# Kernel optimization log

Measured on AMD Instinct MI355X. Metric: run time of the kernel, lower is better.

## Reference

```python
import jax, jax.numpy as jnp
import numpy as np

B, D, N, E = 4, 128, 16384, 65536  # batch, feature_dim, n_junctions, 2*n_lines
EPS = 1e-5  # BatchNorm eps


def setup_inputs() -> dict:
    key = jax.random.key(0)
    ks = jax.random.split(key, 8)
    s = lambda k, shape: jax.random.normal(k, shape, dtype=jnp.float32)
    return {
        "ldesc0": s(ks[0], (B, D, N)),
        "ldesc1": s(ks[1], (B, D, N)),
        "line_enc0": s(ks[2], (B, D, E)),
        "line_enc1": s(ks[3], (B, D, E)),
        "lines_junc_idx0": jax.random.randint(ks[4], (B, E), 0, N),
        "lines_junc_idx1": jax.random.randint(ks[5], (B, E), 0, N),
        # MLP([3D, 2D, D]) params: conv1x1 -> BN -> ReLU -> conv1x1
        "w1": s(ks[6], (2 * D, 3 * D)) * 0.05,
        "b1": jnp.zeros((2 * D,), jnp.float32),
        "bn_gamma": jnp.ones((2 * D,), jnp.float32),
        "bn_beta": jnp.zeros((2 * D,), jnp.float32),
        "bn_mean": jnp.zeros((2 * D,), jnp.float32),
        "bn_var": jnp.ones((2 * D,), jnp.float32),
        "w2": s(ks[7], (D, 2 * D)) * 0.05,
        "b2": jnp.zeros((D,), jnp.float32),
    }


def _mlp(x, w1, b1, g, beta, mu, var, w2, b2):
    # x: [B, 3D, E] -> [B, D, E]; BN in inference mode with running stats
    h = jnp.einsum('oi,bie->boe', w1, x) + b1[None, :, None]
    scale = g / jnp.sqrt(var + EPS)
    h = h * scale[None, :, None] + (beta - mu * scale)[None, :, None]
    h = jax.nn.relu(h)
    return jnp.einsum('oi,bie->boe', w2, h) + b2[None, :, None]


def _endpoint_update(ldesc, line_enc, idx, params):
    # gather endpoint descriptors: [B, D, E]
    line_desc = jax.vmap(lambda x, i: x[:, i])(ldesc, idx)
    b, d, e = line_desc.shape
    # swap the two endpoints of each line (flip along the size-2 axis)
    flipped = line_desc.reshape(b, d, e // 2, 2)[..., ::-1].reshape(b, d, e)
    message = jnp.concatenate([line_desc, flipped, line_enc], axis=1)  # [B, 3D, E]
    return _mlp(message, *params)


def _scatter_mean(src, idx, n):
    # src: [B, D, E], idx: [B, E] -> mean-reduced [B, D, n]; empty slots stay 0
    def one(s, i):
        sums = jax.ops.segment_sum(s.T, i, num_segments=n)                    # [n, D]
        cnt = jax.ops.segment_sum(jnp.ones(s.shape[1], s.dtype), i, num_segments=n)
        return (sums / jnp.maximum(cnt, 1.0)[:, None]).T                      # [D, n]
    return jax.vmap(one)(src, idx)


def reference(ldesc0, ldesc1, line_enc0, line_enc1, lines_junc_idx0, lines_junc_idx1,
              w1, b1, bn_gamma, bn_beta, bn_mean, bn_var, w2, b2):
    params = (w1, b1, bn_gamma, bn_beta, bn_mean, bn_var, w2, b2)
    up0 = _endpoint_update(ldesc0, line_enc0, lines_junc_idx0, params)
    up1 = _endpoint_update(ldesc1, line_enc1, lines_junc_idx1, params)
    n = ldesc0.shape[2]
    out0 = ldesc0 + _scatter_mean(up0, lines_junc_idx0, n)
    out1 = ldesc1 + _scatter_mean(up1, lines_junc_idx1, n)
    return (out0, out1)
```

## Files before the change

### kernel.cpp

```cpp
#include <hip/hip_runtime.h>
#include <hip/hip_bf16.h>
#include <stdint.h>

#define Bb 4
#define Dd 128
#define Nn 16384
#define Ee 65536
#define NTB 16

typedef __attribute__((ext_vector_type(4))) float f32x4;
typedef __attribute__((ext_vector_type(8))) short s16x8;

__device__ __forceinline__ unsigned short f2bf(float f) {
  union { float f; unsigned int u; } v; v.f = f;
  unsigned int r = v.u + 0x7fffu + ((v.u >> 16) & 1u);
  return (unsigned short)(r >> 16);
}

__device__ __forceinline__ unsigned int cvtpk(float lo, float hi) {
  unsigned int r;
  asm volatile("v_cvt_pk_bf16_f32 %0, %1, %2" : "=v"(r) : "v"(lo), "v"(hi));
  return r;
}

__global__ void prep_weights(const float* __restrict__ w1, const float* __restrict__ b1,
                             const float* __restrict__ g, const float* __restrict__ beta,
                             const float* __restrict__ mu, const float* __restrict__ var,
                             const float* __restrict__ w2,
                             unsigned short* __restrict__ W1s, unsigned short* __restrict__ W2s,
                             float* __restrict__ c1) {
  int i = blockIdx.x * 256 + threadIdx.x;
  if (i < 256 * 384) {
    int o = i / 384;
    float scale = g[o] * rsqrtf(var[o] + 1e-5f);
    W1s[i] = f2bf(w1[i] * scale);
  }
  if (i < 128 * 256) W2s[i] = f2bf(w2[i]);
  if (i < 256) {
    float scale = g[i] * rsqrtf(var[i] + 1e-5f);
    c1[i] = b1[i] * scale + beta[i] - mu[i] * scale;
  }
}

__global__ void transpose_ldesc(const float* __restrict__ l0, const float* __restrict__ l1,
                                unsigned short* __restrict__ dst, int side0) {
  __shared__ float tile[32][33];
  int z = blockIdx.z;
  int gs = side0 + (z >> 2), b = z & 3;
  const float* src = (gs ? l1 : l0) + (size_t)b * Dd * Nn;
  unsigned short* d = dst + (size_t)z * Nn * Dd;
  int n0 = blockIdx.x * 32;
  int d0 = blockIdx.y * 32;
  int tx = threadIdx.x, ty = threadIdx.y;
#pragma unroll
  for (int i = 0; i < 4; ++i)
    tile[ty + i * 8][tx] = src[(size_t)(d0 + ty + i * 8) * Nn + n0 + tx];
  __syncthreads();
#pragma unroll
  for (int i = 0; i < 4; ++i) {
    int r = ty + i * 8;
    d[(size_t)(n0 + r) * Dd + d0 + tx] = f2bf(tile[tx][r]);
  }
}

__global__ void hist_kernel(const int* __restrict__ idx0, const int* __restrict__ idx1,
                            int* __restrict__ hist) {
  int i = blockIdx.x * 256 + threadIdx.x;
  int sb = i >> 16;
  int e = i & 65535;
  const int* jx = (sb >= 4) ? idx1 : idx0;
  int n = jx[(size_t)(sb & 3) * Ee + e];
  atomicAdd(&hist[sb * Nn + n], 1);
}

__global__ __launch_bounds__(1024) void scan_kernel(const int* __restrict__ hist,
                                                    int* __restrict__ offs,
                                                    int* __restrict__ cursor) {
  __shared__ int part[1024];
  int sb = blockIdx.x, t = threadIdx.x;
  const int* h = hist + sb * Nn;
  int base = t * 16;
  int v[16];
  int local = 0;
#pragma unroll
  for (int i = 0; i < 16; ++i) { v[i] = local; local += h[base + i]; }
  part[t] = local;
  __syncthreads();
  for (int d = 1; d < 1024; d <<= 1) {
    int y = (t >= d) ? part[t - d] : 0;
    __syncthreads();
    part[t] += y;
    __syncthreads();
  }
  int excl = part[t] - local;
#pragma unroll
  for (int i = 0; i < 16; ++i) {
    int o = excl + v[i];
    offs[sb * Nn + base + i] = o;
    cursor[sb * Nn + base + i] = o;
  }
}

__global__ void fill_kernel(const int* __restrict__ idx0, const int* __restrict__ idx1,
                            int* __restrict__ cursor, int* __restrict__ perm) {
  int i = blockIdx.x * 256 + threadIdx.x;
  int sb = i >> 16;
  int e = i & 65535;
  const int* jx = (sb >= 4) ? idx1 : idx0;
  int n = jx[(size_t)(sb & 3) * Ee + e];
  int pos = atomicAdd(&cursor[sb * Nn + n], 1);
  perm[(size_t)sb * Ee + e] = pos;
}

#define STAGE_DESC(ti, buf)                                                     \
  do {                                                                          \
    int e0s_ = (tile0 + (ti)) * 64;                                             \
    unsigned char* xb_ = sm + (buf) * 32768;                                    \
    int cA_ = w * 8 + (lane >> 4);                                              \
    int cB_ = cA_ + 4;                                                          \
    int uA_ = (lane & 15) ^ (cA_ & 7);                                          \
    int uB_ = (lane & 15) ^ (cB_ & 7);                                          \
    int iA_ = jxB[e0s_ + cA_];                                                  \
    int iB_ = jxB[e0s_ + cB_];                                                  \
    __builtin_amdgcn_global_load_lds(                                           \
        (const __attribute__((address_space(1))) void*)(ldB + ((size_t)iA_) * 128 + uA_ * 8), \
        (__attribute__((address_space(3))) void*)(xb_ + (w * 8) * 256), 16, 0, 0); \
    __builtin_amdgcn_global_load_lds(                                           \
        (const __attribute__((address_space(1))) void*)(ldB + ((size_t)iB_) * 128 + uB_ * 8), \
        (__attribute__((address_space(3))) void*)(xb_ + (w * 8 + 4) * 256), 16, 0, 0); \
  } while (0)

#define ENC_LOAD(ti)                                                            \
  do {                                                                          \
    int e0s_ = (tile0 + (ti)) * 64;                                             \
    const float* es_ = enF + (size_t)(oct * 8) * Ee + e0s_ + ep * 2;            \
    _Pragma("unroll") for (int r = 0; r < 8; ++r)                               \
      ereg[r] = *(const float2*)(es_ + (size_t)r * Ee);                         \
  } while (0)

#define ENC_WRITE(buf)                                                          \
  do {                                                                          \
    unsigned char* xb_ = sm + (buf) * 32768;                                    \
    _Pragma("unroll") for (int j = 0; j < 2; ++j) {                             \
      int e_ = ep * 2 + j;                                                      \
      uint4 pk_;                                                                \
      pk_.x = cvtpk(j ? ereg[0].y : ereg[0].x, j ? ereg[1].y : ereg[1].x);      \
      pk_.y = cvtpk(j ? ereg[2].y : ereg[2].x, j ? ereg[3].y : ereg[3].x);      \
      pk_.z = cvtpk(j ? ereg[4].y : ereg[4].x, j ? ereg[5].y : ereg[5].x);      \
      pk_.w = cvtpk(j ? ereg[6].y : ereg[6].x, j ? ereg[7].y : ereg[7].x);      \
      *(uint4*)(xb_ + 16384 + e_ * 256 + ((oct ^ (e_ & 7)) << 4)) = pk_;        \
    }                                                                           \
  } while (0)

__global__ __launch_bounds__(512, 2) void fused_mlp_ws(
    const unsigned short* __restrict__ ldescT,
    const float* __restrict__ enc0, const float* __restrict__ enc1,
    const int* __restrict__ idx0, const int* __restrict__ idx1, int side0,
    const int* __restrict__ perm,
    const unsigned short* __restrict__ W1s, const unsigned short* __restrict__ W2s,
    const float* __restrict__ c1, const float* __restrict__ b2,
    unsigned short* __restrict__ U) {
  __shared__ __align__(16) unsigned char sm[98304];

  const int t = threadIdx.x;
  const int w = t >> 6;
  const int lane = t & 63;
  const int lr = t & 15;
  const int lk = (t & 63) >> 4;
  const int oct = t >> 5;
  const int ep = t & 31;
  const int ls = blockIdx.x >> 8;
  const int gs = side0 + ls;
  const int bB = (blockIdx.x >> 6) & 3;
  const int tile0 = (blockIdx.x & 63) * NTB;

  const int* jxB = (gs ? idx1 : idx0) + (size_t)bB * Ee;
  const int* permB = perm + ((size_t)(gs * Bb + bB)) * Ee;
  const unsigned short* ldB = ldescT + ((size_t)(ls * Bb + bB)) * Nn * 128;
  const float* enF = (gs ? enc1 : enc0) + (size_t)bB * Dd * Ee;
  unsigned short* UB = U + ((size_t)(ls * Bb + bB)) * Ee * 128;

  s16x8 w1f[2][12];
#pragma unroll
  for (int rt = 0; rt < 2; ++rt)
#pragma unroll
    for (int ks = 0; ks < 12; ++ks)
      w1f[rt][ks] = *(const s16x8*)&W1s[(size_t)(w * 32 + rt * 16 + lr) * 384 + ks * 32 + lk * 8];
  s16x8 w2f[8];
#pragma unroll
  for (int ks = 0; ks < 8; ++ks)
    w2f[ks] = *(const s16x8*)&W2s[(size_t)(w * 16 + lr) * 256 + ks * 32 + lk * 8];
  float c1v[2][4], b2v[4];
#pragma unroll
  for (int rt = 0; rt < 2; ++rt)
#pragma unroll
    for (int r = 0; r < 4; ++r) c1v[rt][r] = c1[w * 32 + rt * 16 + lk * 4 + r];
#pragma unroll
  for (int r = 0; r < 4; ++r) b2v[r] = b2[w * 16 + lk * 4 + r];

  float2 ereg[8];
  unsigned short* hb = (unsigned short*)(sm + 65536);

  STAGE_DESC(0, 0);
  STAGE_DESC(1, 1);
  ENC_LOAD(0);
  asm volatile("s_waitcnt vmcnt(0)" ::: "memory");
  ENC_WRITE(0);
  ENC_LOAD(1);
  asm volatile("s_waitcnt vmcnt(0)" ::: "memory");
  ENC_WRITE(1);
  if (2 < NTB) ENC_LOAD(2);
  asm volatile("s_waitcnt lgkmcnt(0)" ::: "memory");
  __builtin_amdgcn_s_barrier();
  __builtin_amdgcn_sched_barrier(0);

#pragma unroll 1
  for (int i = 0; i < NTB; ++i) {
    const int p = i & 1;
    const unsigned short* xb = (const unsigned short*)(sm + p * 32768);
    const int e0c = (tile0 + i) * 64;

    int prow[4];
#pragma unroll
    for (int ct = 0; ct < 4; ++ct) prow[ct] = permB[e0c + ct * 16 + lr];

    f32x4 acc[2][4] = {};
    __builtin_amdgcn_s_setprio(1);
#pragma unroll
    for (int ks = 0; ks < 12; ++ks) {
      s16x8 bf[4];
#pragma unroll
      for (int ct = 0; ct < 4; ++ct) {
        int c = ct * 16 + lr;
        int off;
        if (ks < 4)      { off = c * 128 + (((ks * 4 + lk) ^ (c & 7)) * 8); }
        else if (ks < 8) { int c2 = c ^ 1; off = c2 * 128 + ((((ks - 4) * 4 + lk) ^ (c2 & 7)) * 8); }
        else             { off = 8192 + c * 128 + ((((ks - 8) * 4 + lk) ^ (c & 7)) * 8); }
        bf[ct] = *(const s16x8*)&xb[off];
      }
#pragma unroll
      for (int rt = 0; rt < 2; ++rt)
#pragma unroll
        for (int ct = 0; ct < 4; ++ct)
          acc[rt][ct] = __builtin_amdgcn_mfma_f32_16x16x32_bf16(w1f[rt][ks], bf[ct], acc[rt][ct], 0, 0, 0);
    }
    __builtin_amdgcn_s_setprio(0);

#pragma unroll
    for (int rt = 0; rt < 2; ++rt) {
      int rowbase = w * 32 + rt * 16 + lk * 4;
      int unitr = rowbase >> 3, inner = rowbase & 7;
#pragma unroll
      for (int ct = 0; ct < 4; ++ct) {
        int col = ct * 16 + lr;
        float v0 = fmaxf(acc[rt][ct][0] + c1v[rt][0], 0.f);
        float v1 = fmaxf(acc[rt][ct][1] + c1v[rt][1], 0.f);
        float v2 = fmaxf(acc[rt][ct][2] + c1v[rt][2], 0.f);
        float v3 = fmaxf(acc[rt][ct][3] + c1v[rt][3], 0.f);
        uint2 pk;
        pk.x = cvtpk(v0, v1);
        pk.y = cvtpk(v2, v3);
        *(uint2*)&hb[col * 256 + ((unitr ^ (col & 7)) * 8) + inner] = pk;
      }
    }
    asm volatile("s_waitcnt lgkmcnt(0)" ::: "memory");
    __builtin_amdgcn_s_barrier();
    __builtin_amdgcn_sched_barrier(0);

    if (i == 0) {
      asm volatile("s_waitcnt vmcnt(4)" ::: "memory");
    } else {
      asm volatile("s_waitcnt vmcnt(8)" ::: "memory");
    }
    if (i + 2 < NTB) {
      ENC_WRITE(p);
      STAGE_DESC(i + 2, p);
    }
    if (i + 3 < NTB) ENC_LOAD(i + 3);

    f32x4 acc2[4] = {};
    __builtin_amdgcn_s_setprio(1);
#pragma unroll
    for (int ks = 0; ks < 8; ++ks) {
      s16x8 bf[4];
#pragma unroll
      for (int ct = 0; ct < 4; ++ct) {
        int c = ct * 16 + lr;
        bf[ct] = *(const s16x8*)&hb[c * 256 + (((ks * 4 + lk) ^ (c & 7)) * 8)];
      }
#pragma unroll
      for (int ct = 0; ct < 4; ++ct)
        acc2[ct] = __builtin_amdgcn_mfma_f32_16x16x32_bf16(w2f[ks], bf[ct], acc2[ct], 0, 0, 0);
    }
    __builtin_amdgcn_s_setprio(0);

#pragma unroll
    for (int ct = 0; ct < 4; ++ct) {
      uint2 pk;
      pk.x = cvtpk(acc2[ct][0] + b2v[0], acc2[ct][1] + b2v[1]);
      pk.y = cvtpk(acc2[ct][2] + b2v[2], acc2[ct][3] + b2v[3]);
      *(uint2*)&UB[(((size_t)prow[ct]) << 7) + w * 16 + lk * 4] = pk;
    }

    if (i + 1 < NTB) {
      asm volatile("s_waitcnt lgkmcnt(0)" ::: "memory");
      __builtin_amdgcn_s_barrier();
      __builtin_amdgcn_sched_barrier(0);
    }
  }
}

__global__ __launch_bounds__(256) void scatter_finalize(
    const unsigned short* __restrict__ U,
    const int* __restrict__ offs, const float* __restrict__ l0,
    const float* __restrict__ l1, float* __restrict__ out, int side0) {
  __shared__ float lsum[64][129];
  const int ls = blockIdx.z;
  const int gs = side0 + ls;
  const int b = blockIdx.y;
  const int n0 = blockIdx.x * 64;
  const int t = threadIdx.x;
  const int w = t >> 6, lane = t & 63;
  const unsigned int* Uu = (const unsigned int*)(U + ((size_t)(ls * Bb + b)) * Ee * 128);
  const int* offs_s = offs + ((size_t)(gs * Bb + b)) * Nn;
  const float* l = (gs ? l1 : l0) + (size_t)b * Dd * Nn;
  float* o = out + ((size_t)(gs * Bb + b)) * Dd * Nn;

#pragma unroll 1
  for (int q = 0; q < 16; ++q) {
    int jj = w * 16 + q;
    int n = n0 + jj;
    int s = offs_s[n];
    int e_end = (n == Nn - 1) ? Ee : offs_s[n + 1];
    float s0 = 0.f, s1 = 0.f;
    for (int k = s; k < e_end; ++k) {
      unsigned int p = Uu[(((size_t)k) << 6) + lane];
      union { unsigned int u; float f; } lo, hi;
      lo.u = p << 16;
      hi.u = p & 0xffff0000u;
      s0 += lo.f;
      s1 += hi.f;
    }
    float inv = (e_end > s) ? 1.0f / (float)(e_end - s) : 0.0f;
    lsum[jj][lane * 2] = s0 * inv;
    lsum[jj][lane * 2 + 1] = s1 * inv;
  }
  __syncthreads();

  int nloc = t & 63;
  int dbase = (t >> 6) * 32;
#pragma unroll
  for (int i = 0; i < 32; ++i) {
    int d = dbase + i;
    size_t off2 = (size_t)d * Nn + n0 + nloc;
    o[off2] = l[off2] + lsum[nloc][d];
  }
}

extern "C" void kernel_launch(void* const* d_in, const int* in_sizes, int n_in,
                              void* d_out, int out_size, void* d_ws, size_t ws_size,
                              hipStream_t stream) {
  const float* ldesc0 = (const float*)d_in[0];
  const float* ldesc1 = (const float*)d_in[1];
  const float* enc0   = (const float*)d_in[2];
  const float* enc1   = (const float*)d_in[3];
  const int*   idx0   = (const int*)d_in[4];
  const int*   idx1   = (const int*)d_in[5];
  const float* w1     = (const float*)d_in[6];
  const float* b1     = (const float*)d_in[7];
  const float* g      = (const float*)d_in[8];
  const float* beta   = (const float*)d_in[9];
  const float* mu     = (const float*)d_in[10];
  const float* var    = (const float*)d_in[11];
  const float* w2     = (const float*)d_in[12];
  const float* b2     = (const float*)d_in[13];
  float* out = (float*)d_out;

  char* ws = (char*)d_ws;
  size_t off = 0;
  unsigned short* W1s = (unsigned short*)(ws + off); off += 256 * 384 * 2;
  unsigned short* W2s = (unsigned short*)(ws + off); off += 128 * 256 * 2;
  float* c1   = (float*)(ws + off); off += 256 * 4;
  int* hist   = (int*)(ws + off); off += (size_t)8 * Nn * 4;
  int* offs   = (int*)(ws + off); off += (size_t)8 * Nn * 4;
  int* cursor = (int*)(ws + off); off += (size_t)8 * Nn * 4;
  int* perm   = (int*)(ws + off); off += (size_t)8 * Ee * 4;
  size_t small_end = off;

  const size_t tside = (size_t)Bb * Nn * Dd * 2;
  const size_t bigside = (size_t)Bb * Ee * Dd * 2;
  size_t need_full = small_end + 2 * tside + 2 * bigside;
  const bool full = (ws_size >= need_full);
  const int sides_buf = full ? 2 : 1;

  unsigned short* t = (unsigned short*)(ws + off); off += tside * sides_buf;
  unsigned short* U = (unsigned short*)(ws + off); off += bigside * sides_buf;

  hipMemsetAsync(hist, 0, (size_t)8 * Nn * 4, stream);
  prep_weights<<<384, 256, 0, stream>>>(w1, b1, g, beta, mu, var, w2, W1s, W2s, c1);
  hist_kernel<<<2048, 256, 0, stream>>>(idx0, idx1, hist);
  scan_kernel<<<8, 1024, 0, stream>>>(hist, offs, cursor);
  fill_kernel<<<2048, 256, 0, stream>>>(idx0, idx1, cursor, perm);

  if (full) {
    transpose_ldesc<<<dim3(Nn / 32, Dd / 32, 8), dim3(32, 8), 0, stream>>>(
        ldesc0, ldesc1, t, 0);
    fused_mlp_ws<<<512, 512, 0, stream>>>(t, enc0, enc1, idx0, idx1, 0, perm,
                                          W1s, W2s, c1, b2, U);
    scatter_finalize<<<dim3(Nn / 64, Bb, 2), 256, 0, stream>>>(
        U, offs, ldesc0, ldesc1, out, 0);
  } else {
    for (int side = 0; side < 2; ++side) {
      transpose_ldesc<<<dim3(Nn / 32, Dd / 32, 4), dim3(32, 8), 0, stream>>>(
          ldesc0, ldesc1, t, side);
      fused_mlp_ws<<<256, 512, 0, stream>>>(t, enc0, enc1, idx0, idx1, side, perm,
                                            W1s, W2s, c1, b2, U);
      scatter_finalize<<<dim3(Nn / 64, Bb, 1), 256, 0, stream>>>(
          U, offs, ldesc0, ldesc1, out, side);
    }
  }
}
```

Baseline: 384.5 us.

## Process tile pairs per barrier in fused MLP and merge weight prep with histogram

The fused MLP kernel now processes two 64-edge tiles per loop iteration. It runs both first GEMMs, then one barrier, then both second GEMMs, using two hidden-activation buffers. This raises shared memory from 96KB to 128KB. Index prefetch is split from the descriptor staging so gather indices load early. The change halves the number of barriers and waitcnt stalls per tile, at the cost of a shallower prefetch (vmcnt(0) waits) and fewer blocks per CU because of the larger LDS footprint. Separately, weight preparation and histogram building are merged into one launch to save a kernel launch.

Measured after the change: 579.8 us. 50.8% more time.

```diff
diff --git a/kernel.cpp b/kernel.cpp
--- a/kernel.cpp
+++ b/kernel.cpp
@@ -23,12 +23,13 @@
   return r;
 }
 
-__global__ void prep_weights(const float* __restrict__ w1, const float* __restrict__ b1,
-                             const float* __restrict__ g, const float* __restrict__ beta,
-                             const float* __restrict__ mu, const float* __restrict__ var,
-                             const float* __restrict__ w2,
-                             unsigned short* __restrict__ W1s, unsigned short* __restrict__ W2s,
-                             float* __restrict__ c1) {
+__global__ void prep_and_hist(const float* __restrict__ w1, const float* __restrict__ b1,
+                              const float* __restrict__ g, const float* __restrict__ beta,
+                              const float* __restrict__ mu, const float* __restrict__ var,
+                              const float* __restrict__ w2,
+                              const int* __restrict__ idx0, const int* __restrict__ idx1,
+                              unsigned short* __restrict__ W1s, unsigned short* __restrict__ W2s,
+                              float* __restrict__ c1, int* __restrict__ hist) {
   int i = blockIdx.x * 256 + threadIdx.x;
   if (i < 256 * 384) {
     int o = i / 384;
@@ -40,6 +41,11 @@
     float scale = g[i] * rsqrtf(var[i] + 1e-5f);
     c1[i] = b1[i] * scale + beta[i] - mu[i] * scale;
   }
+  int sb = i >> 16;
+  int e = i & 65535;
+  const int* jx = (sb >= 4) ? idx1 : idx0;
+  int n = jx[(size_t)(sb & 3) * Ee + e];
+  atomicAdd(&hist[sb * Nn + n], 1);
 }
 
 __global__ void transpose_ldesc(const float* __restrict__ l0, const float* __restrict__ l1,
@@ -63,16 +69,6 @@
   }
 }
 
-__global__ void hist_kernel(const int* __restrict__ idx0, const int* __restrict__ idx1,
-                            int* __restrict__ hist) {
-  int i = blockIdx.x * 256 + threadIdx.x;
-  int sb = i >> 16;
-  int e = i & 65535;
-  const int* jx = (sb >= 4) ? idx1 : idx0;
-  int n = jx[(size_t)(sb & 3) * Ee + e];
-  atomicAdd(&hist[sb * Nn + n], 1);
-}
-
 __global__ __launch_bounds__(1024) void scan_kernel(const int* __restrict__ hist,
                                                     int* __restrict__ offs,
                                                     int* __restrict__ cursor) {
@@ -112,43 +108,106 @@
   perm[(size_t)sb * Ee + e] = pos;
 }
 
-#define STAGE_DESC(ti, buf)                                                     \
-  do {                                                                          \
-    int e0s_ = (tile0 + (ti)) * 64;                                             \
+#define STAGE_DESC_REG(ti, buf, iA_, iB_)                                       \
+  do {                                                                          \
     unsigned char* xb_ = sm + (buf) * 32768;                                    \
     int cA_ = w * 8 + (lane >> 4);                                              \
     int cB_ = cA_ + 4;                                                          \
     int uA_ = (lane & 15) ^ (cA_ & 7);                                          \
     int uB_ = (lane & 15) ^ (cB_ & 7);                                          \
-    int iA_ = jxB[e0s_ + cA_];                                                  \
-    int iB_ = jxB[e0s_ + cB_];                                                  \
     __builtin_amdgcn_global_load_lds(                                           \
-        (const __attribute__((address_space(1))) void*)(ldB + ((size_t)iA_) * 128 + uA_ * 8), \
+        (const __attribute__((address_space(1))) void*)(ldB + ((size_t)(iA_)) * 128 + uA_ * 8), \
         (__attribute__((address_space(3))) void*)(xb_ + (w * 8) * 256), 16, 0, 0); \
     __builtin_amdgcn_global_load_lds(                                           \
-        (const __attribute__((address_space(1))) void*)(ldB + ((size_t)iB_) * 128 + uB_ * 8), \
+        (const __attribute__((address_space(1))) void*)(ldB + ((size_t)(iB_)) * 128 + uB_ * 8), \
         (__attribute__((address_space(3))) void*)(xb_ + (w * 8 + 4) * 256), 16, 0, 0); \
   } while (0)
 
-#define ENC_LOAD(ti)                                                            \
+#define JX_PREF(ti, iA_, iB_)                                                   \
+  do {                                                                          \
+    int e0s_ = (tile0 + (ti)) * 64;                                             \
+    int cA_ = w * 8 + (lane >> 4);                                              \
+    iA_ = jxB[e0s_ + cA_];                                                      \
+    iB_ = jxB[e0s_ + cA_ + 4];                                                  \
+  } while (0)
+
+#define ENC_LOAD(ti, er)                                                        \
   do {                                                                          \
     int e0s_ = (tile0 + (ti)) * 64;                                             \
     const float* es_ = enF + (size_t)(oct * 8) * Ee + e0s_ + ep * 2;            \
     _Pragma("unroll") for (int r = 0; r < 8; ++r)                               \
-      ereg[r] = *(const float2*)(es_ + (size_t)r * Ee);                         \
-  } while (0)
-
-#define ENC_WRITE(buf)                                                          \
+      er[r] = *(const float2*)(es_ + (size_t)r * Ee);                           \
+  } while (0)
+
+#define ENC_WRITE(buf, er)                                                      \
   do {                                                                          \
     unsigned char* xb_ = sm + (buf) * 32768;                                    \
     _Pragma("unroll") for (int j = 0; j < 2; ++j) {                             \
       int e_ = ep * 2 + j;                                                      \
       uint4 pk_;                                                                \
-      pk_.x = cvtpk(j ? ereg[0].y : ereg[0].x, j ? ereg[1].y : ereg[1].x);      \
-      pk_.y = cvtpk(j ? ereg[2].y : ereg[2].x, j ? ereg[3].y : ereg[3].x);      \
-      pk_.z = cvtpk(j ? ereg[4].y : ereg[4].x, j ? ereg[5].y : ereg[5].x);      \
-      pk_.w = cvtpk(j ? ereg[6].y : ereg[6].x, j ? ereg[7].y : ereg[7].x);      \
+      pk_.x = cvtpk(j ? er[0].y : er[0].x, j ? er[1].y : er[1].x);              \
+      pk_.y = cvtpk(j ? er[2].y : er[2].x, j ? er[3].y : er[3].x);              \
+      pk_.z = cvtpk(j ? er[4].y : er[4].x, j ? er[5].y : er[5].x);              \
+      pk_.w = cvtpk(j ? er[6].y : er[6].x, j ? er[7].y : er[7].x);              \
       *(uint4*)(xb_ + 16384 + e_ * 256 + ((oct ^ (e_ & 7)) << 4)) = pk_;        \
+    }                                                                           \
+  } while (0)
+
+#define GEMM1_TILE(xb, hb)                                                      \
+  do {                                                                          \
+    f32x4 acc[2][4] = {};                                                       \
+    __builtin_amdgcn_s_setprio(1);                                              \
+    _Pragma("unroll") for (int ks = 0; ks < 12; ++ks) {                         \
+      s16x8 bf[4];                                                              \
+      _Pragma("unroll") for (int ct = 0; ct < 4; ++ct) {                        \
+        int c = ct * 16 + lr;                                                   \
+        int off;                                                                \
+        if (ks < 4)      { off = c * 128 + (((ks * 4 + lk) ^ (c & 7)) * 8); }   \
+        else if (ks < 8) { int c2 = c ^ 1; off = c2 * 128 + ((((ks - 4) * 4 + lk) ^ (c2 & 7)) * 8); } \
+        else             { off = 8192 + c * 128 + ((((ks - 8) * 4 + lk) ^ (c & 7)) * 8); } \
+        bf[ct] = *(const s16x8*)&(xb)[off];                                     \
+      }                                                                         \
+      _Pragma("unroll") for (int rt = 0; rt < 2; ++rt)                          \
+        _Pragma("unroll") for (int ct = 0; ct < 4; ++ct)                        \
+          acc[rt][ct] = __builtin_amdgcn_mfma_f32_16x16x32_bf16(w1f[rt][ks], bf[ct], acc[rt][ct], 0, 0, 0); \
+    }                                                                           \
+    __builtin_amdgcn_s_setprio(0);                                              \
+    _Pragma("unroll") for (int rt = 0; rt < 2; ++rt) {                          \
+      int rowbase = w * 32 + rt * 16 + lk * 4;                                  \
+      int unitr = rowbase >> 3, inner = rowbase & 7;                            \
+      _Pragma("unroll") for (int ct = 0; ct < 4; ++ct) {                        \
+        int col = ct * 16 + lr;                                                 \
+        float v0 = fmaxf(acc[rt][ct][0] + c1v[rt][0], 0.f);                     \
+        float v1 = fmaxf(acc[rt][ct][1] + c1v[rt][1], 0.f);                     \
+        float v2 = fmaxf(acc[rt][ct][2] + c1v[rt][2], 0.f);                     \
+        float v3 = fmaxf(acc[rt][ct][3] + c1v[rt][3], 0.f);                     \
+        uint2 pk;                                                               \
+        pk.x = cvtpk(v0, v1);                                                   \
+        pk.y = cvtpk(v2, v3);                                                   \
+        *(uint2*)&(hb)[col * 256 + ((unitr ^ (col & 7)) * 8) + inner] = pk;     \
+      }                                                                         \
+    }                                                                           \
+  } while (0)
+
+#define GEMM2_STORE(hb, prw)                                                    \
+  do {                                                                          \
+    f32x4 acc2[4] = {};                                                         \
+    __builtin_amdgcn_s_setprio(1);                                              \
+    _Pragma("unroll") for (int ks = 0; ks < 8; ++ks) {                          \
+      s16x8 bf[4];                                                              \
+      _Pragma("unroll") for (int ct = 0; ct < 4; ++ct) {                        \
+        int c = ct * 16 + lr;                                                   \
+        bf[ct] = *(const s16x8*)&(hb)[c * 256 + (((ks * 4 + lk) ^ (c & 7)) * 8)]; \
+      }                                                                         \
+      _Pragma("unroll") for (int ct = 0; ct < 4; ++ct)                          \
+        acc2[ct] = __builtin_amdgcn_mfma_f32_16x16x32_bf16(w2f[ks], bf[ct], acc2[ct], 0, 0, 0); \
+    }                                                                           \
+    __builtin_amdgcn_s_setprio(0);                                              \
+    _Pragma("unroll") for (int ct = 0; ct < 4; ++ct) {                          \
+      uint2 pk;                                                                 \
+      pk.x = cvtpk(acc2[ct][0] + b2v[0], acc2[ct][1] + b2v[1]);                 \
+      pk.y = cvtpk(acc2[ct][2] + b2v[2], acc2[ct][3] + b2v[3]);                 \
+      *(uint2*)&UB[(((size_t)(prw)[ct]) << 7) + w * 16 + lk * 4] = pk;          \
     }                                                                           \
   } while (0)
 
@@ -160,7 +219,7 @@
     const unsigned short* __restrict__ W1s, const unsigned short* __restrict__ W2s,
     const float* __restrict__ c1, const float* __restrict__ b2,
     unsigned short* __restrict__ U) {
-  __shared__ __align__(16) unsigned char sm[98304];
+  __shared__ __align__(16) unsigned char sm[131072];
 
   const int t = threadIdx.x;
   const int w = t >> 6;
@@ -198,111 +257,73 @@
 #pragma unroll
   for (int r = 0; r < 4; ++r) b2v[r] = b2[w * 16 + lk * 4 + r];
 
-  float2 ereg[8];
-  unsigned short* hb = (unsigned short*)(sm + 65536);
-
-  STAGE_DESC(0, 0);
-  STAGE_DESC(1, 1);
-  ENC_LOAD(0);
+  float2 eregA[8], eregB[8];
+  unsigned short* xb0 = (unsigned short*)sm;
+  unsigned short* xb1 = (unsigned short*)(sm + 32768);
+  unsigned short* hb0 = (unsigned short*)(sm + 65536);
+  unsigned short* hb1 = (unsigned short*)(sm + 98304);
+
+  {
+    int i0A, i0B, i1A, i1B;
+    JX_PREF(0, i0A, i0B);
+    JX_PREF(1, i1A, i1B);
+    STAGE_DESC_REG(0, 0, i0A, i0B);
+    STAGE_DESC_REG(1, 1, i1A, i1B);
+  }
+  ENC_LOAD(0, eregA);
+  ENC_LOAD(1, eregB);
   asm volatile("s_waitcnt vmcnt(0)" ::: "memory");
-  ENC_WRITE(0);
-  ENC_LOAD(1);
-  asm volatile("s_waitcnt vmcnt(0)" ::: "memory");
-  ENC_WRITE(1);
-  if (2 < NTB) ENC_LOAD(2);
+  ENC_WRITE(0, eregA);
+  ENC_WRITE(1, eregB);
   asm volatile("s_waitcnt lgkmcnt(0)" ::: "memory");
   __builtin_amdgcn_s_barrier();
   __builtin_amdgcn_sched_barrier(0);
 
 #pragma unroll 1
-  for (int i = 0; i < NTB; ++i) {
-    const int p = i & 1;
-    const unsigned short* xb = (const unsigned short*)(sm + p * 32768);
-    const int e0c = (tile0 + i) * 64;
-
-    int prow[4];
-#pragma unroll
-    for (int ct = 0; ct < 4; ++ct) prow[ct] = permB[e0c + ct * 16 + lr];
-
-    f32x4 acc[2][4] = {};
-    __builtin_amdgcn_s_setprio(1);
-#pragma unroll
-    for (int ks = 0; ks < 12; ++ks) {
-      s16x8 bf[4];
-#pragma unroll
-      for (int ct = 0; ct < 4; ++ct) {
-        int c = ct * 16 + lr;
-        int off;
-        if (ks < 4)      { off = c * 128 + (((ks * 4 + lk) ^ (c & 7)) * 8); }
-        else if (ks < 8) { int c2 = c ^ 1; off = c2 * 128 + ((((ks - 4) * 4 + lk) ^ (c2 & 7)) * 8); }
-        else             { off = 8192 + c * 128 + ((((ks - 8) * 4 + lk) ^ (c & 7)) * 8); }
-        bf[ct] = *(const s16x8*)&xb[off];
-      }
-#pragma unroll
-      for (int rt = 0; rt < 2; ++rt)
-#pragma unroll
-        for (int ct = 0; ct < 4; ++ct)
-          acc[rt][ct] = __builtin_amdgcn_mfma_f32_16x16x32_bf16(w1f[rt][ks], bf[ct], acc[rt][ct], 0, 0, 0);
-    }
-    __builtin_amdgcn_s_setprio(0);
-
-#pragma unroll
-    for (int rt = 0; rt < 2; ++rt) {
-      int rowbase = w * 32 + rt * 16 + lk * 4;
-      int unitr = rowbase >> 3, inner = rowbase & 7;
-#pragma unroll
-      for (int ct = 0; ct < 4; ++ct) {
-        int col = ct * 16 + lr;
-        float v0 = fmaxf(acc[rt][ct][0] + c1v[rt][0], 0.f);
-        float v1 = fmaxf(acc[rt][ct][1] + c1v[rt][1], 0.f);
-        float v2 = fmaxf(acc[rt][ct][2] + c1v[rt][2], 0.f);
-        float v3 = fmaxf(acc[rt][ct][3] + c1v[rt][3], 0.f);
-        uint2 pk;
-        pk.x = cvtpk(v0, v1);
-        pk.y = cvtpk(v2, v3);
-        *(uint2*)&hb[col * 256 + ((unitr ^ (col & 7)) * 8) + inner] = pk;
-      }
-    }
+  for (int jp = 0; jp < NTB / 2; ++jp) {
+    const int j = jp * 2;
+    const bool more = (j + 2 < NTB);
+    const int e0a = (tile0 + j) * 64;
+    const int e0b = (tile0 + j + 1) * 64;
+
+    int prowA[4], prowB[4];
+#pragma unroll
+    for (int ct = 0; ct < 4; ++ct) {
+      prowA[ct] = permB[e0a + ct * 16 + lr];
+      prowB[ct] = permB[e0b + ct * 16 + lr];
+    }
+    int iA2 = 0, iB2 = 0, iA3 = 0, iB3 = 0;
+    if (more) {
+      JX_PREF(j + 2, iA2, iB2);
+      JX_PREF(j + 3, iA3, iB3);
+      ENC_LOAD(j + 2, eregA);
+      ENC_LOAD(j + 3, eregB);
+    }
+
+    GEMM1_TILE(xb0, hb0);
+    GEMM1_TILE(xb1, hb1);
+
     asm volatile("s_waitcnt lgkmcnt(0)" ::: "memory");
     __builtin_amdgcn_s_barrier();
     __builtin_amdgcn_sched_barrier(0);
 
-    if (i == 0) {
-      asm volatile("s_waitcnt vmcnt(4)" ::: "memory");
+    if (more) {
+      asm volatile("s_waitcnt vmcnt(0)" ::: "memory");
+      __builtin_amdgcn_sched_barrier(0);
+      ENC_WRITE(0, eregA);
+      ENC_WRITE(1, eregB);
+      STAGE_DESC_REG(j + 2, 0, iA2, iB2);
+      STAGE_DESC_REG(j + 3, 1, iA3, iB3);
     } else {
+      asm volatile("s_waitcnt vmcnt(0)" ::: "memory");
+      __builtin_amdgcn_sched_barrier(0);
+    }
+
+    GEMM2_STORE(hb0, prowA);
+    GEMM2_STORE(hb1, prowB);
+
+    if (more) {
       asm volatile("s_waitcnt vmcnt(8)" ::: "memory");
-    }
-    if (i + 2 < NTB) {
-      ENC_WRITE(p);
-      STAGE_DESC(i + 2, p);
-    }
-    if (i + 3 < NTB) ENC_LOAD(i + 3);
-
-    f32x4 acc2[4] = {};
-    __builtin_amdgcn_s_setprio(1);
-#pragma unroll
-    for (int ks = 0; ks < 8; ++ks) {
-      s16x8 bf[4];
-#pragma unroll
-      for (int ct = 0; ct < 4; ++ct) {
-        int c = ct * 16 + lr;
-        bf[ct] = *(const s16x8*)&hb[c * 256 + (((ks * 4 + lk) ^ (c & 7)) * 8)];
-      }
-#pragma unroll
-      for (int ct = 0; ct < 4; ++ct)
-        acc2[ct] = __builtin_amdgcn_mfma_f32_16x16x32_bf16(w2f[ks], bf[ct], acc2[ct], 0, 0, 0);
-    }
-    __builtin_amdgcn_s_setprio(0);
-
-#pragma unroll
-    for (int ct = 0; ct < 4; ++ct) {
-      uint2 pk;
-      pk.x = cvtpk(acc2[ct][0] + b2v[0], acc2[ct][1] + b2v[1]);
-      pk.y = cvtpk(acc2[ct][2] + b2v[2], acc2[ct][3] + b2v[3]);
-      *(uint2*)&UB[(((size_t)prow[ct]) << 7) + w * 16 + lk * 4] = pk;
-    }
-
-    if (i + 1 < NTB) {
       asm volatile("s_waitcnt lgkmcnt(0)" ::: "memory");
       __builtin_amdgcn_s_barrier();
       __builtin_amdgcn_sched_barrier(0);
@@ -397,8 +418,8 @@
   unsigned short* U = (unsigned short*)(ws + off); off += bigside * sides_buf;
 
   hipMemsetAsync(hist, 0, (size_t)8 * Nn * 4, stream);
-  prep_weights<<<384, 256, 0, stream>>>(w1, b1, g, beta, mu, var, w2, W1s, W2s, c1);
-  hist_kernel<<<2048, 256, 0, stream>>>(idx0, idx1, hist);
+  prep_and_hist<<<2048, 256, 0, stream>>>(w1, b1, g, beta, mu, var, w2,
+                                          idx0, idx1, W1s, W2s, c1, hist);
   scan_kernel<<<8, 1024, 0, stream>>>(hist, offs, cursor);
   fill_kernel<<<2048, 256, 0, stream>>>(idx0, idx1, cursor, perm);
 
```
